# Optimization experiments

Hardware: AMD Instinct MI355X
Metric: run time of the kernel (lower is better)

## Reference

```python
import jax, jax.numpy as jnp
import numpy as np

DIM_PROBLEM = 8192
DIM_CONTEXT = 512
DIM_HIDDEN = 1024


def setup_inputs() -> dict:
    key = jax.random.key(0)
    ks = jax.random.split(key, 8)
    s = 0.02
    H, C = DIM_HIDDEN, DIM_CONTEXT
    return {
        "context": jax.random.normal(ks[0], (C,), jnp.float32),
        # linear_1: dim_context -> 1
        "W1": jax.random.normal(ks[1], (1, C), jnp.float32) * s,
        "b1": jnp.zeros((1,), jnp.float32),
        # LSTM layer 0 (input dim 1), torch gate order [i, f, g, o]
        "Wih0": jax.random.normal(ks[2], (4 * H, 1), jnp.float32) * s,
        "Whh0": jax.random.normal(ks[3], (4 * H, H), jnp.float32) * s,
        "bih0": jnp.zeros((4 * H,), jnp.float32),
        "bhh0": jnp.zeros((4 * H,), jnp.float32),
        # LSTM layer 1 (input dim H)
        "Wih1": jax.random.normal(ks[4], (4 * H, H), jnp.float32) * s,
        "Whh1": jax.random.normal(ks[5], (4 * H, H), jnp.float32) * s,
        "bih1": jnp.zeros((4 * H,), jnp.float32),
        "bhh1": jnp.zeros((4 * H,), jnp.float32),
        # linear_2: dim_hidden -> 1
        "W2": jax.random.normal(ks[6], (1, H), jnp.float32) * s,
        "b2": jnp.zeros((1,), jnp.float32),
    }


def _lstm_cell(gin, h, c, Whh, b):
    # gin = W_ih @ x (precomputed); torch gate order i, f, g, o
    gates = gin + Whh @ h + b
    i, f, g, o = jnp.split(gates, 4)
    i, f, o = jax.nn.sigmoid(i), jax.nn.sigmoid(f), jax.nn.sigmoid(o)
    g = jnp.tanh(g)
    c = f * c + i * g
    return o * jnp.tanh(c), c


def reference(context, W1, b1, Wih0, Whh0, bih0, bhh0, Wih1, Whh1, bih1, bhh1, W2, b2):
    H = Whh0.shape[1]
    x0 = (W1 @ context + b1)[0]  # linear_1 seeds the first LSTM input (scalar)
    b0 = bih0 + bhh0
    b1g = bih1 + bhh1
    keys = jax.random.split(jax.random.key(42), DIM_PROBLEM)

    def step(carry, k):
        h0, c0, h1, c1, x, logp = carry
        h0, c0 = _lstm_cell(Wih0[:, 0] * x, h0, c0, Whh0, b0)
        h1, c1 = _lstm_cell(Wih1 @ h0, h1, c1, Whh1, b1g)
        p = jax.nn.sigmoid(W2 @ h1 + b2)[0]
        # Bernoulli sample; detached as in the original (.clone().detach(), .item())
        s = jax.lax.stop_gradient(jax.random.bernoulli(k, p).astype(jnp.float32))
        # log of running product  p^s * (1-p)^(1-s)
        logp = logp + s * jnp.log(p) + (1.0 - s) * jnp.log1p(-p)
        return (h0, c0, h1, c1, s, logp), s

    z = jnp.zeros((H,), jnp.float32)
    carry0 = (z, z, z, z, x0, jnp.float32(0.0))
    (_, _, _, _, _, logp), solution = jax.lax.scan(step, carry0, keys)
    return solution, logp
```

## Files before the change

kernel.cpp:

```cpp
#include <hip/hip_runtime.h>
#include <stdint.h>
#include <math.h>


#define H     1024
#define NSTEP 8192
#define NWG   512
#define BLK   64
#define NROW  25

typedef _Float16 h2 __attribute__((ext_vector_type(2)));
typedef _Float16 h8 __attribute__((ext_vector_type(8)));

union U32H2 { uint32_t u; h2 v; };

__device__ __forceinline__ unsigned long long pack_vt(float v0, float v1, uint32_t tag){
  U32H2 p; p.v.x = (_Float16)v0; p.v.y = (_Float16)v1;
  return ((unsigned long long)tag << 32) | (unsigned long long)p.u;
}

__device__ __forceinline__ void pub_slot(unsigned long long* p, unsigned long long v){
  (void)__hip_atomic_exchange(p, v, __ATOMIC_RELAXED, __HIP_MEMORY_SCOPE_AGENT);
}

__device__ __forceinline__ uint2 tf2x32(uint32_t k0, uint32_t k1, uint32_t x0, uint32_t x1){
  uint32_t k2 = k0 ^ k1 ^ 0x1BD11BDAu;
  x0 += k0; x1 += k1;
#define TFR(r) { x0 += x1; x1 = (x1 << (r)) | (x1 >> (32 - (r))); x1 ^= x0; }
  TFR(13) TFR(15) TFR(26) TFR(6)
  x0 += k1; x1 += k2 + 1u;
  TFR(17) TFR(29) TFR(16) TFR(24)
  x0 += k2; x1 += k0 + 2u;
  TFR(13) TFR(15) TFR(26) TFR(6)
  x0 += k0; x1 += k1 + 3u;
  TFR(17) TFR(29) TFR(16) TFR(24)
  x0 += k1; x1 += k2 + 4u;
  TFR(13) TFR(15) TFR(26) TFR(6)
  x0 += k2; x1 += k0 + 5u;
#undef TFR
  uint2 r; r.x = x0; r.y = x1; return r;
}

__device__ __forceinline__ uint32_t jax_word(uint32_t i){
  return (i < 8192u) ? tf2x32(0u, 42u, i, i + 8192u).x
                     : tf2x32(0u, 42u, i - 8192u, i).y;
}

__device__ __forceinline__ float wred64(float x){
  #pragma unroll
  for(int off = 32; off > 0; off >>= 1) x += __shfl_xor(x, off, 64);
  return x;
}

#if __has_builtin(__builtin_amdgcn_fdot2)
__device__ __forceinline__ float fdot2f(h2 a, h2 b, float c){ return __builtin_amdgcn_fdot2(a, b, c, false); }
#else
__device__ __forceinline__ float fdot2f(h2 a, h2 b, float c){
  return (float)a.x * (float)b.x + (float)a.y * (float)b.y + c;
}
#endif

__device__ __forceinline__ float sigm(float x){
  x = fminf(fmaxf(x, -30.f), 30.f);
  return 1.f / (1.f + __expf(-x));
}
__device__ __forceinline__ float tanh_f(float x){
  x = fminf(fmaxf(x, -15.f), 15.f);
  float e = __expf(2.f * x);
  return (e - 1.f) / (e + 1.f);
}

__device__ __forceinline__ unsigned long long ld_slot(const unsigned long long* p){
  return __hip_atomic_load((unsigned long long*)p, __ATOMIC_RELAXED, __HIP_MEMORY_SCOPE_AGENT);
}

__device__ __forceinline__ unsigned long long spin2(const unsigned long long* p,
                                                    uint32_t tag,
                                                    unsigned long long init){
  if((uint32_t)(init >> 32) == tag) return init;
  unsigned long long a = ld_slot(p);
  unsigned long long b = ld_slot(p);
  while(true){
    if((uint32_t)(a >> 32) == tag) return a;
    a = ld_slot(p);
    if((uint32_t)(b >> 32) == tag) return b;
    b = ld_slot(p);
  }
}

__device__ __forceinline__ void poll_h(const unsigned long long* __restrict__ buf,
                                       uint32_t tag, int lane, h2* hv){
  const unsigned long long* p0 = buf + (lane << 2);
  const unsigned long long* p1 = buf + 256 + (lane << 2);
  unsigned long long pv[8];
  #pragma unroll
  for(int k = 0; k < 4; k++) pv[k]     = ld_slot(p0 + k);
  #pragma unroll
  for(int k = 0; k < 4; k++) pv[4 + k] = ld_slot(p1 + k);

  pv[0] = spin2(p0, tag, pv[0]);

  bool any = false;
  #pragma unroll
  for(int k = 1; k < 8; k++) any |= ((uint32_t)(pv[k] >> 32) != tag);
  if(any){
    #pragma unroll
    for(int k = 1; k < 8; k++){
      if((uint32_t)(pv[k] >> 32) != tag){
        const unsigned long long* p = (k < 4) ? (p0 + k) : (p1 + (k - 4));
        pv[k] = ld_slot(p);
      }
    }
    #pragma unroll
    for(int k = 1; k < 8; k++){
      const unsigned long long* p = (k < 4) ? (p0 + k) : (p1 + (k - 4));
      pv[k] = spin2(p, tag, pv[k]);
    }
  }

  #pragma unroll
  for(int k = 0; k < 8; k++){
    U32H2 u; u.u = (uint32_t)pv[k];
    hv[k] = u.v;
  }
}

__device__ __forceinline__ float row_part(const h2* __restrict__ wrow, int lane, const h2* hv){
  h8 wl = *(const h8*)(wrow + (lane << 2));
  h8 wh = *(const h8*)(wrow + 256 + (lane << 2));
  float a0 = 0.f, a1 = 0.f;
  h2 w;
  w = __builtin_shufflevector(wl, wl, 0, 1); a0 = fdot2f(w, hv[0], a0);
  w = __builtin_shufflevector(wl, wl, 2, 3); a1 = fdot2f(w, hv[1], a1);
  w = __builtin_shufflevector(wl, wl, 4, 5); a0 = fdot2f(w, hv[2], a0);
  w = __builtin_shufflevector(wl, wl, 6, 7); a1 = fdot2f(w, hv[3], a1);
  w = __builtin_shufflevector(wh, wh, 0, 1); a0 = fdot2f(w, hv[4], a0);
  w = __builtin_shufflevector(wh, wh, 2, 3); a1 = fdot2f(w, hv[5], a1);
  w = __builtin_shufflevector(wh, wh, 4, 5); a0 = fdot2f(w, hv[6], a0);
  w = __builtin_shufflevector(wh, wh, 6, 7); a1 = fdot2f(w, hv[7], a1);
  return a0 + a1;
}

__global__ void __launch_bounds__(BLK)
lstm_persist(const float* __restrict__ ctx,  const float* __restrict__ W1p,  const float* __restrict__ b1p,
             const float* __restrict__ Wih0, const float* __restrict__ Whh0,
             const float* __restrict__ bih0, const float* __restrict__ bhh0,
             const float* __restrict__ Wih1, const float* __restrict__ Whh1,
             const float* __restrict__ bih1, const float* __restrict__ bhh1,
             const float* __restrict__ W2p,  const float* __restrict__ b2p,
             float* __restrict__ out,
             unsigned long long* __restrict__ h0buf,
             unsigned long long* __restrict__ h1buf)
{
  __shared__ h2 w[NROW][H/2];

  const int lane = threadIdx.x;
  const int wg   = blockIdx.x;
  const int j0   = wg << 1;

  #pragma unroll 1
  for(int r = 0; r < NROW; r++){
    const float* rowp;
    if(r < 8)      { int g = r & 3,        j = j0 + (r >> 2);        rowp = Wih1 + (size_t)(g*H + j)*H; }
    else if(r < 16){ int rr = r - 8;  int g = rr & 3, j = j0 + (rr >> 2); rowp = Whh0 + (size_t)(g*H + j)*H; }
    else if(r < 24){ int rr = r - 16; int g = rr & 3, j = j0 + (rr >> 2); rowp = Whh1 + (size_t)(g*H + j)*H; }
    else           rowp = W2p;
    const float4* s4 = (const float4*)rowp;
    #pragma unroll
    for(int it = 0; it < 4; it++){
      float4 f = s4[lane + (it << 6)];
      h2 pa; pa.x = (_Float16)f.x; pa.y = (_Float16)f.y;
      h2 pb; pb.x = (_Float16)f.z; pb.y = (_Float16)f.w;
      const int ci = (lane + (it << 6)) << 1;
      w[r][ci] = pa; w[r][ci + 1] = pb;
    }
  }
  __syncthreads();

  float b0g[8], b1g[8], w0g[8];
  #pragma unroll
  for(int e = 0; e < 2; e++){
    const int j = j0 + e;
    #pragma unroll
    for(int g = 0; g < 4; g++){
      b0g[4*e + g] = bih0[g*H + j] + bhh0[g*H + j];
      b1g[4*e + g] = bih1[g*H + j] + bhh1[g*H + j];
      w0g[4*e + g] = Wih0[g*H + j];
    }
  }
  const float b2v = b2p[0];

  float xacc = 0.f;
  for(int c = lane; c < 512; c += 64) xacc += W1p[c] * ctx[c];
  const float x0 = wred64(xacc) + b1p[0];

  float c0[2], c1[2] = {0.f, 0.f}, logp = 0.f;
  float a0[8];
  float a1[8] = {0.f,0.f,0.f,0.f,0.f,0.f,0.f,0.f};

  {
    float h0v[2];
    #pragma unroll
    for(int e = 0; e < 2; e++){
      float gi = sigm (w0g[4*e+0]*x0 + b0g[4*e+0]);
      float gg = tanh_f(w0g[4*e+2]*x0 + b0g[4*e+2]);
      float go = sigm (w0g[4*e+3]*x0 + b0g[4*e+3]);
      c0[e] = gi * gg;
      h0v[e] = go * tanh_f(c0[e]);
    }
    if(lane == 0)
      pub_slot(&h0buf[wg], pack_vt(h0v[0], h0v[1], 1u));
  }

  h2 hv[8];
  float u = 0.f;

  #pragma unroll 1
  for(int t = 0; t < NSTEP; t++){
    const uint32_t tt = (uint32_t)t;

    poll_h(h0buf, tt + 1u, lane, hv);

    float s1[8];
    #pragma unroll
    for(int r = 0; r < 8; r++) s1[r] = row_part(&w[r][0], lane, hv);
    #pragma unroll
    for(int off = 32; off > 0; off >>= 1){
      #pragma unroll
      for(int r = 0; r < 8; r++) s1[r] += __shfl_xor(s1[r], off, 64);
    }
    {
      float h1v[2];
      #pragma unroll
      for(int e = 0; e < 2; e++){
        float gi = sigm (s1[4*e+0] + a1[4*e+0] + b1g[4*e+0]);
        float gf = sigm (s1[4*e+1] + a1[4*e+1] + b1g[4*e+1]);
        float gg = tanh_f(s1[4*e+2] + a1[4*e+2] + b1g[4*e+2]);
        float go = sigm (s1[4*e+3] + a1[4*e+3] + b1g[4*e+3]);
        c1[e] = gf*c1[e] + gi*gg;
        h1v[e] = go * tanh_f(c1[e]);
      }
      if(lane == 0)
        pub_slot(&h1buf[wg], pack_vt(h1v[0], h1v[1], tt + 1u));
    }

    {
      const uint32_t kk0 = jax_word(2u*tt), kk1 = jax_word(2u*tt + 1u);
      const uint32_t bits = tf2x32(kk0, kk1, 0u, 0u).x;
      u = __uint_as_float((bits >> 9) | 0x3f800000u) - 1.0f;
    }
    float sa[8];
    #pragma unroll
    for(int r = 0; r < 8; r++) sa[r] = row_part(&w[8 + r][0], lane, hv);
    #pragma unroll
    for(int off = 32; off > 0; off >>= 1){
      #pragma unroll
      for(int r = 0; r < 8; r++) sa[r] += __shfl_xor(sa[r], off, 64);
    }
    #pragma unroll
    for(int r = 0; r < 8; r++) a0[r] = sa[r];

    poll_h(h1buf, tt + 1u, lane, hv);

    float z = row_part(&w[24][0], lane, hv);
    z = wred64(z) + b2v;
    const float p = sigm(z);
    const float s = (u < p) ? 1.f : 0.f;
    {
      float h0v[2];
      #pragma unroll
      for(int e = 0; e < 2; e++){
        float gi = sigm (a0[4*e+0] + w0g[4*e+0]*s + b0g[4*e+0]);
        float gf = sigm (a0[4*e+1] + w0g[4*e+1]*s + b0g[4*e+1]);
        float gg = tanh_f(a0[4*e+2] + w0g[4*e+2]*s + b0g[4*e+2]);
        float go = sigm (a0[4*e+3] + w0g[4*e+3]*s + b0g[4*e+3]);
        c0[e] = gf*c0[e] + gi*gg;
        h0v[e] = go * tanh_f(c0[e]);
      }
      if(lane == 0)
        pub_slot(&h0buf[wg], pack_vt(h0v[0], h0v[1], tt + 2u));
    }

    logp += s * __logf(p) + (1.f - s) * __logf(1.f - p);
    if(wg == 0 && lane == 0) out[t] = s;

    float sb[8];
    #pragma unroll
    for(int r = 0; r < 8; r++) sb[r] = row_part(&w[16 + r][0], lane, hv);
    #pragma unroll
    for(int off = 32; off > 0; off >>= 1){
      #pragma unroll
      for(int r = 0; r < 8; r++) sb[r] += __shfl_xor(sb[r], off, 64);
    }
    #pragma unroll
    for(int r = 0; r < 8; r++) a1[r] = sb[r];
  }

  if(wg == 0 && lane == 0) out[NSTEP] = logp;
}

extern "C" void kernel_launch(void* const* d_in, const int* in_sizes, int n_in,
                              void* d_out, int out_size, void* d_ws, size_t ws_size,
                              hipStream_t stream){
  unsigned long long* h0buf = (unsigned long long*)d_ws;
  unsigned long long* h1buf = h0buf + 512;
  hipLaunchKernelGGL(lstm_persist, dim3(NWG), dim3(BLK), 0, stream,
    (const float*)d_in[0],  (const float*)d_in[1],  (const float*)d_in[2],
    (const float*)d_in[3],  (const float*)d_in[4],  (const float*)d_in[5],  (const float*)d_in[6],
    (const float*)d_in[7],  (const float*)d_in[8],  (const float*)d_in[9],  (const float*)d_in[10],
    (const float*)d_in[11], (const float*)d_in[12],
    (float*)d_out, h0buf, h1buf);
}
```

Measured before the change: 32.97 ms.

## Speculate both sample outcomes to merge two grid syncs per step into one

Each step now computes both possible layer-0 hidden states (sample=0 and sample=1) and publishes them together with h1 in a single packed record per unit. Every workgroup then needs only one cross-workgroup poll per timestep instead of two, and selects the correct branch locally once it has computed the sample. The cost is doubled layer-0 gate math, wider records (16 slots per lane polled), and 16-bit tags in a double-buffered exchange area.

```diff
diff --git a/kernel.cpp b/kernel.cpp
--- a/kernel.cpp
+++ b/kernel.cpp
@@ -14,14 +14,23 @@
 
 union U32H2 { uint32_t u; h2 v; };
 
-__device__ __forceinline__ unsigned long long pack_vt(float v0, float v1, uint32_t tag){
+__device__ __forceinline__ uint16_t f16b(float x){
+  union { _Float16 h; uint16_t u; } c; c.h = (_Float16)x; return c.u;
+}
+
+__device__ __forceinline__ unsigned long long pack_rec(float h1v, float hA, float hB, uint32_t tag){
+  return  (unsigned long long)f16b(h1v)
+       | ((unsigned long long)f16b(hA)  << 16)
+       | ((unsigned long long)f16b(hB)  << 32)
+       | ((unsigned long long)(tag & 0xFFFFu) << 48);
+}
+
+__device__ __forceinline__ unsigned long long pack_boot(float v0, float v1, uint32_t tag){
   U32H2 p; p.v.x = (_Float16)v0; p.v.y = (_Float16)v1;
-  return ((unsigned long long)tag << 32) | (unsigned long long)p.u;
-}
-
-__device__ __forceinline__ void pub_slot(unsigned long long* p, unsigned long long v){
-  (void)__hip_atomic_exchange(p, v, __ATOMIC_RELAXED, __HIP_MEMORY_SCOPE_AGENT);
-}
+  return (unsigned long long)p.u | ((unsigned long long)(tag & 0xFFFFu) << 48);
+}
+
+__device__ __forceinline__ uint32_t rtag(unsigned long long v){ return (uint32_t)(v >> 48); }
 
 __device__ __forceinline__ uint2 tf2x32(uint32_t k0, uint32_t k1, uint32_t x0, uint32_t x1){
   uint32_t k2 = k0 ^ k1 ^ 0x1BD11BDAu;
@@ -73,40 +82,67 @@
 __device__ __forceinline__ unsigned long long ld_slot(const unsigned long long* p){
   return __hip_atomic_load((unsigned long long*)p, __ATOMIC_RELAXED, __HIP_MEMORY_SCOPE_AGENT);
 }
+__device__ __forceinline__ void st_slot(unsigned long long* p, unsigned long long v){
+  __hip_atomic_store(p, v, __ATOMIC_RELAXED, __HIP_MEMORY_SCOPE_AGENT);
+}
 
 __device__ __forceinline__ unsigned long long spin2(const unsigned long long* p,
                                                     uint32_t tag,
                                                     unsigned long long init){
-  if((uint32_t)(init >> 32) == tag) return init;
+  if(rtag(init) == tag) return init;
   unsigned long long a = ld_slot(p);
   unsigned long long b = ld_slot(p);
   while(true){
-    if((uint32_t)(a >> 32) == tag) return a;
+    if(rtag(a) == tag) return a;
     a = ld_slot(p);
-    if((uint32_t)(b >> 32) == tag) return b;
+    if(rtag(b) == tag) return b;
     b = ld_slot(p);
   }
 }
 
-__device__ __forceinline__ void poll_h(const unsigned long long* __restrict__ buf,
-                                       uint32_t tag, int lane, h2* hv){
+__device__ __forceinline__ void poll16(const unsigned long long* __restrict__ buf,
+                                       uint32_t tag, int lane, unsigned long long* pv){
+  const unsigned long long* p0 = buf + (lane << 3);
+  const unsigned long long* p1 = buf + 512 + (lane << 3);
+  #pragma unroll
+  for(int k = 0; k < 8; k++){ pv[k] = ld_slot(p0 + k); pv[8 + k] = ld_slot(p1 + k); }
+
+  pv[0] = spin2(p0, tag, pv[0]);
+
+  bool any = false;
+  #pragma unroll
+  for(int k = 1; k < 16; k++) any |= (rtag(pv[k]) != tag);
+  if(any){
+    #pragma unroll
+    for(int k = 1; k < 16; k++){
+      if(rtag(pv[k]) != tag){
+        const unsigned long long* p = (k < 8) ? (p0 + k) : (p1 + (k - 8));
+        pv[k] = ld_slot(p);
+      }
+    }
+    #pragma unroll
+    for(int k = 1; k < 16; k++){
+      const unsigned long long* p = (k < 8) ? (p0 + k) : (p1 + (k - 8));
+      pv[k] = spin2(p, tag, pv[k]);
+    }
+  }
+}
+
+__device__ __forceinline__ void poll_boot(const unsigned long long* __restrict__ buf,
+                                          uint32_t tag, int lane, h2* hv){
   const unsigned long long* p0 = buf + (lane << 2);
   const unsigned long long* p1 = buf + 256 + (lane << 2);
   unsigned long long pv[8];
   #pragma unroll
-  for(int k = 0; k < 4; k++) pv[k]     = ld_slot(p0 + k);
-  #pragma unroll
-  for(int k = 0; k < 4; k++) pv[4 + k] = ld_slot(p1 + k);
-
+  for(int k = 0; k < 4; k++){ pv[k] = ld_slot(p0 + k); pv[4 + k] = ld_slot(p1 + k); }
   pv[0] = spin2(p0, tag, pv[0]);
-
   bool any = false;
   #pragma unroll
-  for(int k = 1; k < 8; k++) any |= ((uint32_t)(pv[k] >> 32) != tag);
+  for(int k = 1; k < 8; k++) any |= (rtag(pv[k]) != tag);
   if(any){
     #pragma unroll
     for(int k = 1; k < 8; k++){
-      if((uint32_t)(pv[k] >> 32) != tag){
+      if(rtag(pv[k]) != tag){
         const unsigned long long* p = (k < 4) ? (p0 + k) : (p1 + (k - 4));
         pv[k] = ld_slot(p);
       }
@@ -117,12 +153,8 @@
       pv[k] = spin2(p, tag, pv[k]);
     }
   }
-
-  #pragma unroll
-  for(int k = 0; k < 8; k++){
-    U32H2 u; u.u = (uint32_t)pv[k];
-    hv[k] = u.v;
-  }
+  #pragma unroll
+  for(int k = 0; k < 8; k++){ U32H2 u; u.u = (uint32_t)pv[k]; hv[k] = u.v; }
 }
 
 __device__ __forceinline__ float row_part(const h2* __restrict__ wrow, int lane, const h2* hv){
@@ -149,8 +181,8 @@
              const float* __restrict__ bih1, const float* __restrict__ bhh1,
              const float* __restrict__ W2p,  const float* __restrict__ b2p,
              float* __restrict__ out,
-             unsigned long long* __restrict__ h0buf,
-             unsigned long long* __restrict__ h1buf)
+             unsigned long long* __restrict__ h0boot,
+             unsigned long long* __restrict__ ab)
 {
   __shared__ h2 w[NROW][H/2];
 
@@ -195,8 +227,7 @@
   const float x0 = wred64(xacc) + b1p[0];
 
   float c0[2], c1[2] = {0.f, 0.f}, logp = 0.f;
-  float a0[8];
-  float a1[8] = {0.f,0.f,0.f,0.f,0.f,0.f,0.f,0.f};
+  float c0A[2], c0B[2];
 
   {
     float h0v[2];
@@ -209,91 +240,141 @@
       h0v[e] = go * tanh_f(c0[e]);
     }
     if(lane == 0)
-      pub_slot(&h0buf[wg], pack_vt(h0v[0], h0v[1], 1u));
-  }
-
-  h2 hv[8];
-  float u = 0.f;
+      st_slot(&h0boot[wg], pack_boot(h0v[0], h0v[1], 1u));
+  }
+
+  h2 hv0[8], hv1[8];
+  poll_boot(h0boot, 1u, lane, hv0);
+
+  {
+    float rr[16];
+    #pragma unroll
+    for(int r = 0; r < 8; r++) rr[r]     = row_part(&w[r][0],     lane, hv0);
+    #pragma unroll
+    for(int r = 0; r < 8; r++) rr[8 + r] = row_part(&w[8 + r][0], lane, hv0);
+    #pragma unroll
+    for(int off = 32; off > 0; off >>= 1){
+      #pragma unroll
+      for(int r = 0; r < 16; r++) rr[r] += __shfl_xor(rr[r], off, 64);
+    }
+    float h1v[2], hA[2], hB[2];
+    #pragma unroll
+    for(int e = 0; e < 2; e++){
+      float gi = sigm (rr[4*e+0] + b1g[4*e+0]);
+      float gf = sigm (rr[4*e+1] + b1g[4*e+1]);
+      float gg = tanh_f(rr[4*e+2] + b1g[4*e+2]);
+      float go = sigm (rr[4*e+3] + b1g[4*e+3]);
+      c1[e] = gf*c1[e] + gi*gg;
+      h1v[e] = go * tanh_f(c1[e]);
+      float a0c = rr[8+4*e+0], a1c = rr[8+4*e+1], a2c = rr[8+4*e+2], a3c = rr[8+4*e+3];
+      float giA = sigm (a0c + b0g[4*e+0]);
+      float gfA = sigm (a1c + b0g[4*e+1]);
+      float ggA = tanh_f(a2c + b0g[4*e+2]);
+      float goA = sigm (a3c + b0g[4*e+3]);
+      c0A[e] = gfA*c0[e] + giA*ggA; hA[e] = goA * tanh_f(c0A[e]);
+      float giB = sigm (a0c + w0g[4*e+0] + b0g[4*e+0]);
+      float gfB = sigm (a1c + w0g[4*e+1] + b0g[4*e+1]);
+      float ggB = tanh_f(a2c + w0g[4*e+2] + b0g[4*e+2]);
+      float goB = sigm (a3c + w0g[4*e+3] + b0g[4*e+3]);
+      c0B[e] = gfB*c0[e] + giB*ggB; hB[e] = goB * tanh_f(c0B[e]);
+    }
+    if(lane == 0){
+      unsigned long long* wb = ab + 1024;
+      st_slot(wb + 2*wg,     pack_rec(h1v[0], hA[0], hB[0], 1u));
+      st_slot(wb + 2*wg + 1, pack_rec(h1v[1], hA[1], hB[1], 1u));
+    }
+  }
+
+  float u;
+  {
+    const uint32_t kk0 = jax_word(0u), kk1 = jax_word(1u);
+    const uint32_t bits = tf2x32(kk0, kk1, 0u, 0u).x;
+    u = __uint_as_float((bits >> 9) | 0x3f800000u) - 1.0f;
+  }
 
   #pragma unroll 1
   for(int t = 0; t < NSTEP; t++){
-    const uint32_t tt = (uint32_t)t;
-
-    poll_h(h0buf, tt + 1u, lane, hv);
-
-    float s1[8];
-    #pragma unroll
-    for(int r = 0; r < 8; r++) s1[r] = row_part(&w[r][0], lane, hv);
+    const uint32_t tau = (uint32_t)t + 1u;
+
+    const unsigned long long* bp = ab + ((size_t)(tau & 1u) << 10);
+    unsigned long long pv[16];
+    poll16(bp, tau, lane, pv);
+
+    #pragma unroll
+    for(int k = 0; k < 8; k++){
+      U32H2 uu;
+      uu.u = ((uint32_t)pv[2*k] & 0xFFFFu) | (((uint32_t)pv[2*k+1] & 0xFFFFu) << 16);
+      hv1[k] = uu.v;
+    }
+
+    float z = row_part(&w[24][0], lane, hv1);
+    z = wred64(z) + b2v;
+    const float p = sigm(z);
+    const float sv = (u < p) ? 1.f : 0.f;
+    const bool sb = (sv != 0.f);
+
+    const uint32_t sh = sb ? 32u : 16u;
+    #pragma unroll
+    for(int k = 0; k < 8; k++){
+      U32H2 uu;
+      uu.u = ((uint32_t)(pv[2*k] >> sh) & 0xFFFFu)
+           | (((uint32_t)(pv[2*k+1] >> sh) & 0xFFFFu) << 16);
+      hv0[k] = uu.v;
+    }
+    #pragma unroll
+    for(int e = 0; e < 2; e++) c0[e] = sb ? c0B[e] : c0A[e];
+
+    float rr[24];
+    #pragma unroll
+    for(int r = 0; r < 8; r++) rr[r]      = row_part(&w[r][0],      lane, hv0);
+    #pragma unroll
+    for(int r = 0; r < 8; r++) rr[8 + r]  = row_part(&w[8 + r][0],  lane, hv0);
+    #pragma unroll
+    for(int r = 0; r < 8; r++) rr[16 + r] = row_part(&w[16 + r][0], lane, hv1);
     #pragma unroll
     for(int off = 32; off > 0; off >>= 1){
       #pragma unroll
-      for(int r = 0; r < 8; r++) s1[r] += __shfl_xor(s1[r], off, 64);
-    }
+      for(int r = 0; r < 24; r++) rr[r] += __shfl_xor(rr[r], off, 64);
+    }
+
     {
-      float h1v[2];
+      float h1v[2], hA[2], hB[2];
       #pragma unroll
       for(int e = 0; e < 2; e++){
-        float gi = sigm (s1[4*e+0] + a1[4*e+0] + b1g[4*e+0]);
-        float gf = sigm (s1[4*e+1] + a1[4*e+1] + b1g[4*e+1]);
-        float gg = tanh_f(s1[4*e+2] + a1[4*e+2] + b1g[4*e+2]);
-        float go = sigm (s1[4*e+3] + a1[4*e+3] + b1g[4*e+3]);
+        float gi = sigm (rr[4*e+0] + rr[16+4*e+0] + b1g[4*e+0]);
+        float gf = sigm (rr[4*e+1] + rr[16+4*e+1] + b1g[4*e+1]);
+        float gg = tanh_f(rr[4*e+2] + rr[16+4*e+2] + b1g[4*e+2]);
+        float go = sigm (rr[4*e+3] + rr[16+4*e+3] + b1g[4*e+3]);
         c1[e] = gf*c1[e] + gi*gg;
         h1v[e] = go * tanh_f(c1[e]);
+
+        float a0c = rr[8+4*e+0], a1c = rr[8+4*e+1], a2c = rr[8+4*e+2], a3c = rr[8+4*e+3];
+        float giA = sigm (a0c + b0g[4*e+0]);
+        float gfA = sigm (a1c + b0g[4*e+1]);
+        float ggA = tanh_f(a2c + b0g[4*e+2]);
+        float goA = sigm (a3c + b0g[4*e+3]);
+        c0A[e] = gfA*c0[e] + giA*ggA; hA[e] = goA * tanh_f(c0A[e]);
+        float giB = sigm (a0c + w0g[4*e+0] + b0g[4*e+0]);
+        float gfB = sigm (a1c + w0g[4*e+1] + b0g[4*e+1]);
+        float ggB = tanh_f(a2c + w0g[4*e+2] + b0g[4*e+2]);
+        float goB = sigm (a3c + w0g[4*e+3] + b0g[4*e+3]);
+        c0B[e] = gfB*c0[e] + giB*ggB; hB[e] = goB * tanh_f(c0B[e]);
       }
-      if(lane == 0)
-        pub_slot(&h1buf[wg], pack_vt(h1v[0], h1v[1], tt + 1u));
-    }
-
+      if(lane == 0){
+        unsigned long long* wb = ab + ((size_t)((tau + 1u) & 1u) << 10);
+        st_slot(wb + 2*wg,     pack_rec(h1v[0], hA[0], hB[0], tau + 1u));
+        st_slot(wb + 2*wg + 1, pack_rec(h1v[1], hA[1], hB[1], tau + 1u));
+      }
+    }
+
+    logp += sv * __logf(p) + (1.f - sv) * __logf(1.f - p);
+    if(wg == 0 && lane == 0) out[t] = sv;
     {
-      const uint32_t kk0 = jax_word(2u*tt), kk1 = jax_word(2u*tt + 1u);
+      const uint32_t tn = (uint32_t)t + 1u;
+      const uint32_t kk0 = jax_word(2u*tn), kk1 = jax_word(2u*tn + 1u);
       const uint32_t bits = tf2x32(kk0, kk1, 0u, 0u).x;
       u = __uint_as_float((bits >> 9) | 0x3f800000u) - 1.0f;
     }
-    float sa[8];
-    #pragma unroll
-    for(int r = 0; r < 8; r++) sa[r] = row_part(&w[8 + r][0], lane, hv);
-    #pragma unroll
-    for(int off = 32; off > 0; off >>= 1){
-      #pragma unroll
-      for(int r = 0; r < 8; r++) sa[r] += __shfl_xor(sa[r], off, 64);
-    }
-    #pragma unroll
-    for(int r = 0; r < 8; r++) a0[r] = sa[r];
-
-    poll_h(h1buf, tt + 1u, lane, hv);
-
-    float z = row_part(&w[24][0], lane, hv);
-    z = wred64(z) + b2v;
-    const float p = sigm(z);
-    const float s = (u < p) ? 1.f : 0.f;
-    {
-      float h0v[2];
-      #pragma unroll
-      for(int e = 0; e < 2; e++){
-        float gi = sigm (a0[4*e+0] + w0g[4*e+0]*s + b0g[4*e+0]);
-        float gf = sigm (a0[4*e+1] + w0g[4*e+1]*s + b0g[4*e+1]);
-        float gg = tanh_f(a0[4*e+2] + w0g[4*e+2]*s + b0g[4*e+2]);
-        float go = sigm (a0[4*e+3] + w0g[4*e+3]*s + b0g[4*e+3]);
-        c0[e] = gf*c0[e] + gi*gg;
-        h0v[e] = go * tanh_f(c0[e]);
-      }
-      if(lane == 0)
-        pub_slot(&h0buf[wg], pack_vt(h0v[0], h0v[1], tt + 2u));
-    }
-
-    logp += s * __logf(p) + (1.f - s) * __logf(1.f - p);
-    if(wg == 0 && lane == 0) out[t] = s;
-
-    float sb[8];
-    #pragma unroll
-    for(int r = 0; r < 8; r++) sb[r] = row_part(&w[16 + r][0], lane, hv);
-    #pragma unroll
-    for(int off = 32; off > 0; off >>= 1){
-      #pragma unroll
-      for(int r = 0; r < 8; r++) sb[r] += __shfl_xor(sb[r], off, 64);
-    }
-    #pragma unroll
-    for(int r = 0; r < 8; r++) a1[r] = sb[r];
   }
 
   if(wg == 0 && lane == 0) out[NSTEP] = logp;
@@ -302,12 +383,13 @@
 extern "C" void kernel_launch(void* const* d_in, const int* in_sizes, int n_in,
                               void* d_out, int out_size, void* d_ws, size_t ws_size,
                               hipStream_t stream){
-  unsigned long long* h0buf = (unsigned long long*)d_ws;
-  unsigned long long* h1buf = h0buf + 512;
+  unsigned long long* ws = (unsigned long long*)d_ws;
+  unsigned long long* h0boot = ws;
+  unsigned long long* ab     = ws + 512;
   hipLaunchKernelGGL(lstm_persist, dim3(NWG), dim3(BLK), 0, stream,
     (const float*)d_in[0],  (const float*)d_in[1],  (const float*)d_in[2],
     (const float*)d_in[3],  (const float*)d_in[4],  (const float*)d_in[5],  (const float*)d_in[6],
     (const float*)d_in[7],  (const float*)d_in[8],  (const float*)d_in[9],  (const float*)d_in[10],
     (const float*)d_in[11], (const float*)d_in[12],
-    (float*)d_out, h0buf, h1buf);
-}
+    (float*)d_out, h0boot, ab);
+}
```

Measured after the change: 62.58 ms. +89.8%, slower.
